# Kernel tuning notes

Hardware: AMD Instinct MI355X
Metric: run time of the kernel (lower is better)

## Reference

```python
import jax, jax.numpy as jnp
import numpy as np
import math

B, S, HID = 2, 2048, 2048
NH, NKV = 32, 8
HD = HID // NH  # 64
N_REP = NH // NKV  # 4


def setup_inputs() -> dict:
    key = jax.random.key(0)
    ks = jax.random.split(key, 7)
    sc = 0.02
    return {
        "hidden_states": jax.random.normal(ks[0], (B, S, HID), jnp.float32),
        "cos": jax.random.normal(ks[1], (S, HD), jnp.float32),
        "sin": jax.random.normal(ks[2], (S, HD), jnp.float32),
        "wq": jax.random.normal(ks[3], (NH * HD, HID), jnp.float32) * sc,
        "wk": jax.random.normal(ks[4], (NKV * HD, HID), jnp.float32) * sc,
        "wv": jax.random.normal(ks[5], (NKV * HD, HID), jnp.float32) * sc,
        "wo": jax.random.normal(ks[6], (HID, NH * HD), jnp.float32) * sc,
    }


def _rotate_half(x):
    x1, x2 = jnp.split(x, 2, axis=-1)
    return jnp.concatenate([-x2, x1], axis=-1)


def _apply_rotary(q, k, cos, sin):
    # q: [B,S,NH,HD], k: [B,S,NKV,HD]; cos/sin: [S,HD] broadcast over batch, heads
    c = cos[None, :, None, :]
    s = sin[None, :, None, :]
    return q * c + _rotate_half(q) * s, k * c + _rotate_half(k) * s


def reference(hidden_states, cos, sin, wq, wk, wv, wo):
    x = hidden_states  # [B,S,HID]
    q = jnp.einsum('bsh,dh->bsd', x, wq).reshape(B, S, NH, HD)
    k = jnp.einsum('bsh,dh->bsd', x, wk).reshape(B, S, NKV, HD)
    v = jnp.einsum('bsh,dh->bsd', x, wv).reshape(B, S, NKV, HD)
    q, k = _apply_rotary(q, k, cos, sin)
    # repeat_kv: expand kv heads by N_REP -> [B,S,NH,HD]
    k = jnp.repeat(k, N_REP, axis=2)
    v = jnp.repeat(v, N_REP, axis=2)
    # [B,NH,S,HD]
    q = q.transpose(0, 2, 1, 3)
    k = k.transpose(0, 2, 1, 3)
    v = v.transpose(0, 2, 1, 3)
    scores = jnp.einsum('bhqd,bhkd->bhqk', q, k) / math.sqrt(HD)
    probs = jax.nn.softmax(scores.astype(jnp.float32), axis=-1).astype(q.dtype)
    out = jnp.einsum('bhqk,bhkd->bhqd', probs, v)
    out = out.transpose(0, 2, 1, 3).reshape(B, S, NH * HD)
    return jnp.einsum('bsd,hd->bsh', out, wo)
```

## Files before the change

### kernel.cpp

```cpp
#include <hip/hip_runtime.h>
#include <math.h>

#define B 2
#define S 2048
#define HID 2048
#define NH 32
#define NKV 8
#define HD 64
#define NREP 4

typedef __bf16 bf16_t;
typedef bf16_t bf16x8 __attribute__((ext_vector_type(8)));
typedef bf16_t bf16x2 __attribute__((ext_vector_type(2)));
typedef float floatx4 __attribute__((ext_vector_type(4)));

__device__ __forceinline__ void gld_lds16(const void* g, void* l) {
    __builtin_amdgcn_global_load_lds(
        (const __attribute__((address_space(1))) void*)g,
        (__attribute__((address_space(3))) void*)l, 16, 0, 0);
}

__device__ __forceinline__ int pack2(float a, float b) {
    bf16x2 v; v[0] = (bf16_t)a; v[1] = (bf16_t)b;
    return __builtin_bit_cast(int, v);
}

__global__ __launch_bounds__(256) void cast_all(const float* __restrict__ x,
                                                const float* __restrict__ wq,
                                                const float* __restrict__ wk,
                                                const float* __restrict__ wv,
                                                const float* __restrict__ wo,
                                                bf16_t* __restrict__ xb,
                                                bf16_t* __restrict__ wqkvb,
                                                bf16_t* __restrict__ wob) {
    int gid = blockIdx.x * 256 + threadIdx.x;
    const float* src; bf16_t* dst; int idx;
    if (gid < 1048576)      { src = x;  dst = xb;               idx = gid; }
    else if (gid < 1572864) { src = wq; dst = wqkvb;            idx = gid - 1048576; }
    else if (gid < 1703936) { src = wk; dst = wqkvb + 4194304;  idx = gid - 1572864; }
    else if (gid < 1835008) { src = wv; dst = wqkvb + 5242880;  idx = gid - 1703936; }
    else                    { src = wo; dst = wob;              idx = gid - 1835008; }
    size_t i = (size_t)idx * 8;
    float4 f0 = *(const float4*)(src + i);
    float4 f1 = *(const float4*)(src + i + 4);
    bf16x8 v;
    v[0] = (bf16_t)f0.x; v[1] = (bf16_t)f0.y; v[2] = (bf16_t)f0.z; v[3] = (bf16_t)f0.w;
    v[4] = (bf16_t)f1.x; v[5] = (bf16_t)f1.y; v[6] = (bf16_t)f1.z; v[7] = (bf16_t)f1.w;
    *(bf16x8*)(dst + i) = v;
}

#define TM 128
#define TN 128
#define BK 64

enum { MODE_QKV = 0, MODE_OUT = 2 };

template <int MODE>
__global__ __launch_bounds__(256) void gemm_mfma(const bf16_t* __restrict__ A,
                                                 const bf16_t* __restrict__ W,
                                                 void* __restrict__ outQ,
                                                 bf16_t* __restrict__ outK,
                                                 bf16_t* __restrict__ outV,
                                                 const float* __restrict__ cosp,
                                                 const float* __restrict__ sinp,
                                                 int M, int N, int K) {
    __shared__ __align__(16) bf16_t As[2 * TM * 32];
    __shared__ __align__(16) bf16_t Ws[2 * TN * 32];
    const int t    = threadIdx.x;
    const int wave = t >> 6, lane = t & 63;
    const int quad = lane >> 4, l16 = lane & 15;
    const int m0 = blockIdx.y * TM, n0 = blockIdx.x * TN;
    const int wm = (wave >> 1) * 64, wn = (wave & 1) * 64;

    floatx4 zero4 = {0.f, 0.f, 0.f, 0.f};
    floatx4 acc[4][4];
    #pragma unroll
    for (int i = 0; i < 4; ++i)
        #pragma unroll
        for (int j = 0; j < 4; ++j) acc[i][j] = zero4;

    const int r4 = t >> 2;
    const int c8 = (t & 3) * 8;
    const bf16_t* Arow = A + (size_t)(m0 + r4) * K + c8;
    const bf16_t* Wrow = W + (size_t)(n0 + r4) * K + c8;

    for (int k0 = 0; k0 < K; k0 += BK) {
        #pragma unroll
        for (int ks = 0; ks < 2; ++ks) {
            gld_lds16(Arow + k0 + ks * 32,          As + ks * 4096 + t * 8);
            gld_lds16(Arow + 64 * K + k0 + ks * 32, As + ks * 4096 + 2048 + t * 8);
            gld_lds16(Wrow + k0 + ks * 32,          Ws + ks * 4096 + t * 8);
            gld_lds16(Wrow + 64 * K + k0 + ks * 32, Ws + ks * 4096 + 2048 + t * 8);
        }
        __syncthreads();
        #pragma unroll
        for (int ks = 0; ks < 2; ++ks) {
            bf16x8 af[4], bfr[4];
            #pragma unroll
            for (int i = 0; i < 4; ++i)
                af[i] = *(bf16x8*)&As[ks * 4096 + (wm + i * 16 + l16) * 32 + quad * 8];
            #pragma unroll
            for (int j = 0; j < 4; ++j)
                bfr[j] = *(bf16x8*)&Ws[ks * 4096 + (wn + j * 16 + l16) * 32 + quad * 8];
            #pragma unroll
            for (int i = 0; i < 4; ++i)
                #pragma unroll
                for (int j = 0; j < 4; ++j)
                    acc[i][j] = __builtin_amdgcn_mfma_f32_16x16x32_bf16(af[i], bfr[j], acc[i][j], 0, 0, 0);
        }
        __syncthreads();
    }

    if constexpr (MODE == MODE_OUT) {
        float* C = (float*)outQ;
        #pragma unroll
        for (int i = 0; i < 4; ++i)
            #pragma unroll
            for (int r = 0; r < 4; ++r) {
                int row = m0 + wm + i * 16 + quad * 4 + r;
                #pragma unroll
                for (int j = 0; j < 4; ++j)
                    C[(size_t)row * N + n0 + wn + j * 16 + l16] = acc[i][j][r];
            }
    } else {
        const int hh = (n0 + wn) / 64;
        #pragma unroll
        for (int i = 0; i < 4; ++i)
            #pragma unroll
            for (int r = 0; r < 4; ++r) {
                int m = m0 + wm + i * 16 + quad * 4 + r;
                int b = m / S, s = m % S;
                if (hh < NH + NKV) {
                    bf16_t* base;
                    float sc;
                    if (hh < NH) {
                        base = (bf16_t*)outQ + ((size_t)(b * NH + hh) * S + s) * HD;
                        sc = 0.18033688011f;
                    } else {
                        base = outK + ((size_t)(b * NKV + (hh - NH)) * S + s) * HD;
                        sc = 1.0f;
                    }
                    #pragma unroll
                    for (int j = 0; j < 2; ++j) {
                        int d = j * 16 + l16;
                        float x1 = acc[i][j][r], x2 = acc[i][j + 2][r];
                        float c1 = cosp[s * HD + d],      s1 = sinp[s * HD + d];
                        float c2 = cosp[s * HD + d + 32], s2 = sinp[s * HD + d + 32];
                        base[d]      = (bf16_t)((x1 * c1 - x2 * s1) * sc);
                        base[d + 32] = (bf16_t)((x2 * c2 + x1 * s2) * sc);
                    }
                } else {
                    int kvh = hh - NH - NKV;
                    bf16_t* vb = outV + ((size_t)(b * NKV + kvh) * HD) * S + s;
                    #pragma unroll
                    for (int j = 0; j < 4; ++j)
                        vb[(size_t)(j * 16 + l16) * S] = (bf16_t)acc[i][j][r];
                }
            }
    }
}

#define PP 72
__global__ __launch_bounds__(128, 2) void attn_mfma(const bf16_t* __restrict__ Q,
                                                    const bf16_t* __restrict__ Kb,
                                                    const bf16_t* __restrict__ Vt,
                                                    bf16_t* __restrict__ Ob) {
    __shared__ __align__(16) bf16_t Ks[2 * 64 * 32];
    __shared__ __align__(16) bf16_t Vs[2 * 64 * 32];
    __shared__ __align__(16) bf16_t Pq[2 * 64 * PP];
    const int t    = threadIdx.x;
    const int wave = t >> 6, lane = t & 63;
    const int quad = lane >> 4, l16 = lane & 15;

    const int flat  = blockIdx.y * 16 + blockIdx.x;
    const int local = flat >> 3;
    const int combo = (flat & 7) * 2 + (local >> 6);
    const int b = combo >> 3, kvh = combo & 7;
    const int h  = kvh * NREP + ((local >> 4) & 3);
    const int q0 = (local & 15) * 128;
    const int bh = b * NH + h;

    const bf16_t* qbase = Q + ((size_t)bh * S + q0 + wave * 64) * HD;
    const bf16_t* kbase = Kb + ((size_t)(b * NKV + kvh) * S) * HD;
    const bf16_t* vbase = Vt + (size_t)(b * NKV + kvh) * HD * S;
    bf16_t* Pqw = Pq + wave * 64 * PP;

    bf16x8 qf[4][2];
    #pragma unroll
    for (int qj = 0; qj < 4; ++qj)
        #pragma unroll
        for (int ks = 0; ks < 2; ++ks)
            qf[qj][ks] = *(const bf16x8*)(qbase + (size_t)(qj * 16 + l16) * HD + ks * 32 + quad * 8);

    floatx4 zero4 = {0.f, 0.f, 0.f, 0.f};
    floatx4 of[4][4];
    #pragma unroll
    for (int di = 0; di < 4; ++di)
        #pragma unroll
        for (int qj = 0; qj < 4; ++qj) of[di][qj] = zero4;
    float lsum[4] = {0.f, 0.f, 0.f, 0.f};

    const int r4 = t >> 2;
    const int c8 = (t & 3) * 8;

    #pragma unroll
    for (int ks = 0; ks < 2; ++ks) {
        gld_lds16(kbase + (size_t)r4 * HD + ks * 32 + c8,        Ks + ks * 2048 + t * 8);
        gld_lds16(kbase + (size_t)(32 + r4) * HD + ks * 32 + c8, Ks + ks * 2048 + 1024 + t * 8);
    }
    __syncthreads();

    for (int kt = 0; kt < S; kt += 64) {
        #pragma unroll
        for (int ks = 0; ks < 2; ++ks) {
            gld_lds16(vbase + (size_t)r4 * S + kt + ks * 32 + c8,        Vs + ks * 2048 + t * 8);
            gld_lds16(vbase + (size_t)(32 + r4) * S + kt + ks * 32 + c8, Vs + ks * 2048 + 1024 + t * 8);
        }
        #pragma unroll
        for (int ki = 0; ki < 4; ++ki) {
            bf16x8 ka0 = *(bf16x8*)&Ks[0 * 2048 + (ki * 16 + l16) * 32 + quad * 8];
            bf16x8 ka1 = *(bf16x8*)&Ks[1 * 2048 + (ki * 16 + l16) * 32 + quad * 8];
            floatx4 sf[4];
            #pragma unroll
            for (int qj = 0; qj < 4; ++qj) sf[qj] = zero4;
            __builtin_amdgcn_s_setprio(1);
            #pragma unroll
            for (int qj = 0; qj < 4; ++qj)
                sf[qj] = __builtin_amdgcn_mfma_f32_16x16x32_bf16(ka0, qf[qj][0], sf[qj], 0, 0, 0);
            #pragma unroll
            for (int qj = 0; qj < 4; ++qj)
                sf[qj] = __builtin_amdgcn_mfma_f32_16x16x32_bf16(ka1, qf[qj][1], sf[qj], 0, 0, 0);
            __builtin_amdgcn_s_setprio(0);
            #pragma unroll
            for (int qj = 0; qj < 4; ++qj) {
                float p0 = __builtin_amdgcn_exp2f(sf[qj][0]);
                float p1 = __builtin_amdgcn_exp2f(sf[qj][1]);
                float p2 = __builtin_amdgcn_exp2f(sf[qj][2]);
                float p3 = __builtin_amdgcn_exp2f(sf[qj][3]);
                lsum[qj] += (p0 + p1) + (p2 + p3);
                int2 pk; pk.x = pack2(p0, p1); pk.y = pack2(p2, p3);
                *(int2*)&Pqw[(qj * 16 + l16) * PP + ki * 16 + quad * 4] = pk;
            }
        }
        __syncthreads();

        if (kt + 64 < S) {
            #pragma unroll
            for (int ks = 0; ks < 2; ++ks) {
                gld_lds16(kbase + (size_t)(kt + 64 + r4) * HD + ks * 32 + c8,      Ks + ks * 2048 + t * 8);
                gld_lds16(kbase + (size_t)(kt + 96 + r4) * HD + ks * 32 + c8,      Ks + ks * 2048 + 1024 + t * 8);
            }
        }
        #pragma unroll
        for (int ks = 0; ks < 2; ++ks) {
            bf16x8 pb[4], va[4];
            #pragma unroll
            for (int qj = 0; qj < 4; ++qj)
                pb[qj] = *(bf16x8*)&Pqw[(qj * 16 + l16) * PP + ks * 32 + quad * 8];
            #pragma unroll
            for (int di = 0; di < 4; ++di)
                va[di] = *(bf16x8*)&Vs[ks * 2048 + (di * 16 + l16) * 32 + quad * 8];
            __builtin_amdgcn_s_setprio(1);
            #pragma unroll
            for (int di = 0; di < 4; ++di)
                #pragma unroll
                for (int qj = 0; qj < 4; ++qj)
                    of[di][qj] = __builtin_amdgcn_mfma_f32_16x16x32_bf16(va[di], pb[qj], of[di][qj], 0, 0, 0);
            __builtin_amdgcn_s_setprio(0);
        }
        __syncthreads();
    }

    #pragma unroll
    for (int qj = 0; qj < 4; ++qj) {
        float ls = lsum[qj];
        ls += __shfl_xor(ls, 16);
        ls += __shfl_xor(ls, 32);
        float inv = 1.f / ls;
        int q = q0 + wave * 64 + qj * 16 + l16;
        bf16_t* ob = Ob + ((size_t)(b * S + q)) * HID + h * HD;
        #pragma unroll
        for (int di = 0; di < 4; ++di) {
            int2 pk;
            pk.x = pack2(of[di][qj][0] * inv, of[di][qj][1] * inv);
            pk.y = pack2(of[di][qj][2] * inv, of[di][qj][3] * inv);
            *(int2*)(ob + di * 16 + quad * 4) = pk;
        }
    }
}

extern "C" void kernel_launch(void* const* d_in, const int* in_sizes, int n_in,
                              void* d_out, int out_size, void* d_ws, size_t ws_size,
                              hipStream_t stream) {
    const float* x    = (const float*)d_in[0];
    const float* cosp = (const float*)d_in[1];
    const float* sinp = (const float*)d_in[2];
    const float* wq   = (const float*)d_in[3];
    const float* wk   = (const float*)d_in[4];
    const float* wv   = (const float*)d_in[5];
    const float* wo   = (const float*)d_in[6];
    float* out = (float*)d_out;

    char* ws = (char*)d_ws;
    bf16_t* xb    = (bf16_t*)(ws);
    bf16_t* kb    = (bf16_t*)(ws + 16777216);
    bf16_t* vtb   = (bf16_t*)(ws + 20971520);
    bf16_t* wqkvb = (bf16_t*)(ws + 25165824);
    bf16_t* wob   = (bf16_t*)(ws + 37748736);
    bf16_t* attb  = (bf16_t*)(ws);
    bf16_t* qb    = (bf16_t*)d_out;

    const int M = B * S;

    cast_all<<<9216, 256, 0, stream>>>(x, wq, wk, wv, wo, xb, wqkvb, wob);

    gemm_mfma<MODE_QKV><<<dim3(3072 / TN, M / TM), 256, 0, stream>>>(
        xb, wqkvb, (void*)qb, kb, vtb, cosp, sinp, M, 3072, HID);

    attn_mfma<<<dim3(S / 128, B * NH), 128, 0, stream>>>(qb, kb, vtb, attb);

    gemm_mfma<MODE_OUT><<<dim3(2048 / TN, M / TM), 256, 0, stream>>>(
        attb, wob, (void*)out, nullptr, nullptr, nullptr, nullptr, M, 2048, HID);
}
```

Baseline: 317.5 us.

## Keep attention probabilities in registers and use four waves of 32 queries

The attention kernel no longer writes the exp'd scores to an LDS P buffer and reads them back. The score MFMA output layout is reused directly as the B operand of the PV MFMA, with V loaded in a matching permuted split-half order. The block grows from 2 to 4 waves, each handling 32 queries instead of 64, so K/V tile loads are shared across more waves and fewer registers are needed per wave. This removes LDS traffic and the shared-memory footprint for P, but each wave now does less MFMA work per K/V tile and the V reads become two 8-byte loads per fragment.

```diff
diff --git a/kernel.cpp b/kernel.cpp
--- a/kernel.cpp
+++ b/kernel.cpp
@@ -11,6 +11,7 @@
 
 typedef __bf16 bf16_t;
 typedef bf16_t bf16x8 __attribute__((ext_vector_type(8)));
+typedef bf16_t bf16x4 __attribute__((ext_vector_type(4)));
 typedef bf16_t bf16x2 __attribute__((ext_vector_type(2)));
 typedef float floatx4 __attribute__((ext_vector_type(4)));
 
@@ -23,6 +24,17 @@
 __device__ __forceinline__ int pack2(float a, float b) {
     bf16x2 v; v[0] = (bf16_t)a; v[1] = (bf16_t)b;
     return __builtin_bit_cast(int, v);
+}
+
+__device__ __forceinline__ bf16x8 cat8(bf16x4 lo, bf16x4 hi) {
+    int2 a = __builtin_bit_cast(int2, lo), b = __builtin_bit_cast(int2, hi);
+    int4 w; w.x = a.x; w.y = a.y; w.z = b.x; w.w = b.y;
+    return __builtin_bit_cast(bf16x8, w);
+}
+
+__device__ __forceinline__ bf16x8 cat8i(int2 lo, int2 hi) {
+    int4 w; w.x = lo.x; w.y = lo.y; w.z = hi.x; w.w = hi.y;
+    return __builtin_bit_cast(bf16x8, w);
 }
 
 __global__ __launch_bounds__(256) void cast_all(const float* __restrict__ x,
@@ -160,14 +172,12 @@
     }
 }
 
-#define PP 72
-__global__ __launch_bounds__(128, 2) void attn_mfma(const bf16_t* __restrict__ Q,
+__global__ __launch_bounds__(256, 4) void attn_mfma(const bf16_t* __restrict__ Q,
                                                     const bf16_t* __restrict__ Kb,
                                                     const bf16_t* __restrict__ Vt,
                                                     bf16_t* __restrict__ Ob) {
     __shared__ __align__(16) bf16_t Ks[2 * 64 * 32];
     __shared__ __align__(16) bf16_t Vs[2 * 64 * 32];
-    __shared__ __align__(16) bf16_t Pq[2 * 64 * PP];
     const int t    = threadIdx.x;
     const int wave = t >> 6, lane = t & 63;
     const int quad = lane >> 4, l16 = lane & 15;
@@ -180,111 +190,105 @@
     const int q0 = (local & 15) * 128;
     const int bh = b * NH + h;
 
-    const bf16_t* qbase = Q + ((size_t)bh * S + q0 + wave * 64) * HD;
+    const bf16_t* qbase = Q + ((size_t)bh * S + q0 + wave * 32) * HD;
     const bf16_t* kbase = Kb + ((size_t)(b * NKV + kvh) * S) * HD;
     const bf16_t* vbase = Vt + (size_t)(b * NKV + kvh) * HD * S;
-    bf16_t* Pqw = Pq + wave * 64 * PP;
-
-    bf16x8 qf[4][2];
-    #pragma unroll
-    for (int qj = 0; qj < 4; ++qj)
+
+    bf16x8 qf[2][2];
+    #pragma unroll
+    for (int qj = 0; qj < 2; ++qj)
         #pragma unroll
         for (int ks = 0; ks < 2; ++ks)
             qf[qj][ks] = *(const bf16x8*)(qbase + (size_t)(qj * 16 + l16) * HD + ks * 32 + quad * 8);
 
     floatx4 zero4 = {0.f, 0.f, 0.f, 0.f};
-    floatx4 of[4][4];
+    floatx4 of[4][2];
     #pragma unroll
     for (int di = 0; di < 4; ++di)
         #pragma unroll
-        for (int qj = 0; qj < 4; ++qj) of[di][qj] = zero4;
-    float lsum[4] = {0.f, 0.f, 0.f, 0.f};
+        for (int qj = 0; qj < 2; ++qj) of[di][qj] = zero4;
+    float lsum[2] = {0.f, 0.f};
 
     const int r4 = t >> 2;
     const int c8 = (t & 3) * 8;
 
     #pragma unroll
-    for (int ks = 0; ks < 2; ++ks) {
-        gld_lds16(kbase + (size_t)r4 * HD + ks * 32 + c8,        Ks + ks * 2048 + t * 8);
-        gld_lds16(kbase + (size_t)(32 + r4) * HD + ks * 32 + c8, Ks + ks * 2048 + 1024 + t * 8);
-    }
+    for (int ks = 0; ks < 2; ++ks)
+        gld_lds16(kbase + (size_t)r4 * HD + ks * 32 + c8, Ks + ks * 2048 + t * 8);
     __syncthreads();
 
     for (int kt = 0; kt < S; kt += 64) {
         #pragma unroll
-        for (int ks = 0; ks < 2; ++ks) {
-            gld_lds16(vbase + (size_t)r4 * S + kt + ks * 32 + c8,        Vs + ks * 2048 + t * 8);
-            gld_lds16(vbase + (size_t)(32 + r4) * S + kt + ks * 32 + c8, Vs + ks * 2048 + 1024 + t * 8);
-        }
+        for (int ks = 0; ks < 2; ++ks)
+            gld_lds16(vbase + (size_t)r4 * S + kt + ks * 32 + c8, Vs + ks * 2048 + t * 8);
+
+        int2 pk[4][2];
         #pragma unroll
         for (int ki = 0; ki < 4; ++ki) {
             bf16x8 ka0 = *(bf16x8*)&Ks[0 * 2048 + (ki * 16 + l16) * 32 + quad * 8];
             bf16x8 ka1 = *(bf16x8*)&Ks[1 * 2048 + (ki * 16 + l16) * 32 + quad * 8];
-            floatx4 sf[4];
-            #pragma unroll
-            for (int qj = 0; qj < 4; ++qj) sf[qj] = zero4;
+            floatx4 sf[2];
+            #pragma unroll
+            for (int qj = 0; qj < 2; ++qj) sf[qj] = zero4;
             __builtin_amdgcn_s_setprio(1);
             #pragma unroll
-            for (int qj = 0; qj < 4; ++qj)
+            for (int qj = 0; qj < 2; ++qj)
                 sf[qj] = __builtin_amdgcn_mfma_f32_16x16x32_bf16(ka0, qf[qj][0], sf[qj], 0, 0, 0);
             #pragma unroll
-            for (int qj = 0; qj < 4; ++qj)
+            for (int qj = 0; qj < 2; ++qj)
                 sf[qj] = __builtin_amdgcn_mfma_f32_16x16x32_bf16(ka1, qf[qj][1], sf[qj], 0, 0, 0);
             __builtin_amdgcn_s_setprio(0);
             #pragma unroll
-            for (int qj = 0; qj < 4; ++qj) {
+            for (int qj = 0; qj < 2; ++qj) {
                 float p0 = __builtin_amdgcn_exp2f(sf[qj][0]);
                 float p1 = __builtin_amdgcn_exp2f(sf[qj][1]);
                 float p2 = __builtin_amdgcn_exp2f(sf[qj][2]);
                 float p3 = __builtin_amdgcn_exp2f(sf[qj][3]);
                 lsum[qj] += (p0 + p1) + (p2 + p3);
-                int2 pk; pk.x = pack2(p0, p1); pk.y = pack2(p2, p3);
-                *(int2*)&Pqw[(qj * 16 + l16) * PP + ki * 16 + quad * 4] = pk;
+                pk[ki][qj].x = pack2(p0, p1);
+                pk[ki][qj].y = pack2(p2, p3);
             }
         }
         __syncthreads();
 
         if (kt + 64 < S) {
             #pragma unroll
-            for (int ks = 0; ks < 2; ++ks) {
-                gld_lds16(kbase + (size_t)(kt + 64 + r4) * HD + ks * 32 + c8,      Ks + ks * 2048 + t * 8);
-                gld_lds16(kbase + (size_t)(kt + 96 + r4) * HD + ks * 32 + c8,      Ks + ks * 2048 + 1024 + t * 8);
+            for (int ks = 0; ks < 2; ++ks)
+                gld_lds16(kbase + (size_t)(kt + 64 + r4) * HD + ks * 32 + c8, Ks + ks * 2048 + t * 8);
+        }
+        #pragma unroll
+        for (int ks = 0; ks < 2; ++ks) {
+            __builtin_amdgcn_s_setprio(1);
+            #pragma unroll
+            for (int di = 0; di < 4; ++di) {
+                bf16x4 vlo = *(bf16x4*)&Vs[ks * 2048 + (di * 16 + l16) * 32 + quad * 4];
+                bf16x4 vhi = *(bf16x4*)&Vs[ks * 2048 + (di * 16 + l16) * 32 + 16 + quad * 4];
+                bf16x8 va = cat8(vlo, vhi);
+                #pragma unroll
+                for (int qj = 0; qj < 2; ++qj) {
+                    bf16x8 pb = cat8i(pk[2 * ks][qj], pk[2 * ks + 1][qj]);
+                    of[di][qj] = __builtin_amdgcn_mfma_f32_16x16x32_bf16(va, pb, of[di][qj], 0, 0, 0);
+                }
             }
-        }
-        #pragma unroll
-        for (int ks = 0; ks < 2; ++ks) {
-            bf16x8 pb[4], va[4];
-            #pragma unroll
-            for (int qj = 0; qj < 4; ++qj)
-                pb[qj] = *(bf16x8*)&Pqw[(qj * 16 + l16) * PP + ks * 32 + quad * 8];
-            #pragma unroll
-            for (int di = 0; di < 4; ++di)
-                va[di] = *(bf16x8*)&Vs[ks * 2048 + (di * 16 + l16) * 32 + quad * 8];
-            __builtin_amdgcn_s_setprio(1);
-            #pragma unroll
-            for (int di = 0; di < 4; ++di)
-                #pragma unroll
-                for (int qj = 0; qj < 4; ++qj)
-                    of[di][qj] = __builtin_amdgcn_mfma_f32_16x16x32_bf16(va[di], pb[qj], of[di][qj], 0, 0, 0);
             __builtin_amdgcn_s_setprio(0);
         }
         __syncthreads();
     }
 
     #pragma unroll
-    for (int qj = 0; qj < 4; ++qj) {
+    for (int qj = 0; qj < 2; ++qj) {
         float ls = lsum[qj];
         ls += __shfl_xor(ls, 16);
         ls += __shfl_xor(ls, 32);
         float inv = 1.f / ls;
-        int q = q0 + wave * 64 + qj * 16 + l16;
+        int q = q0 + wave * 32 + qj * 16 + l16;
         bf16_t* ob = Ob + ((size_t)(b * S + q)) * HID + h * HD;
         #pragma unroll
         for (int di = 0; di < 4; ++di) {
-            int2 pk;
-            pk.x = pack2(of[di][qj][0] * inv, of[di][qj][1] * inv);
-            pk.y = pack2(of[di][qj][2] * inv, of[di][qj][3] * inv);
-            *(int2*)(ob + di * 16 + quad * 4) = pk;
+            int2 pkv;
+            pkv.x = pack2(of[di][qj][0] * inv, of[di][qj][1] * inv);
+            pkv.y = pack2(of[di][qj][2] * inv, of[di][qj][3] * inv);
+            *(int2*)(ob + di * 16 + quad * 4) = pkv;
         }
     }
 }
@@ -317,7 +321,7 @@
     gemm_mfma<MODE_QKV><<<dim3(3072 / TN, M / TM), 256, 0, stream>>>(
         xb, wqkvb, (void*)qb, kb, vtb, cosp, sinp, M, 3072, HID);
 
-    attn_mfma<<<dim3(S / 128, B * NH), 128, 0, stream>>>(qb, kb, vtb, attb);
+    attn_mfma<<<dim3(S / 128, B * NH), 256, 0, stream>>>(qb, kb, vtb, attb);
 
     gemm_mfma<MODE_OUT><<<dim3(2048 / TN, M / TM), 256, 0, stream>>>(
         attb, wob, (void*)out, nullptr, nullptr, nullptr, nullptr, M, 2048, HID);
```

Result: slower. 364.4 us (+14.8%).
